# Optimization experiments

Measured on AMD Instinct MI355X. Metric: run time of the kernel, lower is better.

Reference implementation:

```python
import jax, jax.numpy as jnp
import numpy as np

B, N, D = 4, 1024, 1024      # batch, seq_len, query_dim
H, DH = 16, 64               # heads, dim_head; inner = H*DH = 1024
INNER = H * DH
SCALE = DH ** -0.5


def setup_inputs() -> dict:
    key = jax.random.key(0)
    ks = jax.random.split(key, 8)
    x = jax.random.normal(ks[0], (B, N, D), dtype=jnp.float32)
    rel_pos = jax.random.normal(ks[1], (B * H, N, N), dtype=jnp.float32)
    query_mask = jax.random.randint(ks[2], (B, N), 0, 2).astype(bool)
    context_mask = jax.random.randint(ks[3], (B, N), 0, 2).astype(bool)
    # Linear weights stored (in, out); to_q/to_kv have no bias, to_out has bias.
    Wq = jax.random.normal(ks[4], (D, INNER), dtype=jnp.float32) / np.sqrt(D)
    Wkv = jax.random.normal(ks[5], (D, 2 * INNER), dtype=jnp.float32) / np.sqrt(D)
    Wo = jax.random.normal(ks[6], (INNER, D), dtype=jnp.float32) / np.sqrt(INNER)
    bo = jax.random.normal(ks[7], (D,), dtype=jnp.float32) * 0.01
    return {"x": x, "rel_pos": rel_pos, "query_mask": query_mask,
            "context_mask": context_mask, "Wq": Wq, "Wkv": Wkv, "Wo": Wo, "bo": bo}


def reference(x, rel_pos, query_mask, context_mask, Wq, Wkv, Wo, bo):
    # Self-attention (context = x)
    q = x @ Wq                                 # [B, N, INNER]
    kv = x @ Wkv                               # [B, N, 2*INNER]
    k, v = jnp.split(kv, 2, axis=-1)
    # (b n (h d)) -> (b h n d)
    split_heads = lambda t: t.reshape(B, N, H, DH).transpose(0, 2, 1, 3)
    q, k, v = map(split_heads, (q, k, v))
    sim = jnp.einsum('bhid,bhjd->bhij', q, k) * SCALE
    sim = sim + rel_pos.reshape(B, H, N, N)
    neg = -jnp.finfo(sim.dtype).max
    # query_mask: (b i) -> mask rows; context_mask: (b j) -> mask cols
    sim = jnp.where(query_mask[:, None, :, None], sim, neg)
    sim = jnp.where(context_mask[:, None, None, :], sim, neg)
    attn = jax.nn.softmax(sim, axis=-1)
    out = jnp.einsum('bhij,bhjd->bhid', attn, v)    # [B, H, N, DH]
    out = out.transpose(0, 2, 1, 3).reshape(B, N, INNER)
    return out @ Wo + bo
```

## Files before the change

### kernel.cpp

```cpp
#include <hip/hip_runtime.h>


#define NEGMAX 3.402823466e+38f

typedef short short8 __attribute__((ext_vector_type(8)));
typedef float f32x4 __attribute__((ext_vector_type(4)));

__device__ __forceinline__ unsigned short f2bf(float f) {
  unsigned int u = __float_as_uint(f);
  u += 0x7FFFu + ((u >> 16) & 1u);
  return (unsigned short)(u >> 16);
}

__device__ __forceinline__ void stage16(const void* g, void* lds_base, int lane) {
#if __has_builtin(__builtin_amdgcn_global_load_lds)
  __builtin_amdgcn_global_load_lds(
      (const __attribute__((address_space(1))) unsigned int*)g,
      (__attribute__((address_space(3))) unsigned int*)lds_base, 16, 0, 0);
#else
  *(int4*)((char*)lds_base + lane * 16) = *(const int4*)g;
#endif
}

__global__ void cast_x_k(const float* __restrict__ x, unsigned short* __restrict__ xb) {
  int i = (blockIdx.x * 256 + threadIdx.x) * 4;
  float4 v = *(const float4*)(x + i);
  ushort4 o;
  o.x = f2bf(v.x); o.y = f2bf(v.y); o.z = f2bf(v.z); o.w = f2bf(v.w);
  *(ushort4*)(xb + i) = o;
}

__global__ __launch_bounds__(256) void tcast_k(const float* __restrict__ src, int ldsrc,
                                               unsigned short* __restrict__ dst) {
  __shared__ float T[64][65];
  const int n0 = blockIdx.x * 64, d0 = blockIdx.y * 64;
  const int tx = threadIdx.x & 63, ty = threadIdx.x >> 6;
#pragma unroll
  for (int k = 0; k < 16; ++k) {
    int dl = k * 4 + ty;
    T[dl][tx] = src[(size_t)(d0 + dl) * ldsrc + n0 + tx];
  }
  __syncthreads();
#pragma unroll
  for (int k = 0; k < 16; ++k) {
    int nl = k * 4 + ty;
    dst[(size_t)(n0 + nl) * 1024 + d0 + tx] = f2bf(T[tx][nl]);
  }
}

__global__ __launch_bounds__(256) void gemm_bt_k(
    const unsigned short* __restrict__ A, const unsigned short* __restrict__ Bt,
    unsigned short* __restrict__ qws, unsigned short* __restrict__ kws,
    unsigned short* __restrict__ vtws) {
  constexpr int K = 1024;
  constexpr int NKB = K / 32;
  __shared__ alignas(16) unsigned short As[128 * 32];
  __shared__ alignas(16) unsigned short Bs[128 * 32];
  const int tid = threadIdx.x;
  const int lane = tid & 63, w = tid >> 6;
  const int quad = lane >> 4, lanelo = lane & 15;
  const int tRow = blockIdx.y * 128, tCol = blockIdx.x * 128;
  const int wr = (w >> 1) * 64, wc = (w & 1) * 64;
  const char* AgB = (const char*)(A + (size_t)tRow * K);
  const char* BgB = (const char*)(Bt + (size_t)tCol * K);
  const int c0 = tid, c1 = tid + 256;
  const size_t a0off = (size_t)(c0 >> 2) * 2048 + (c0 & 3) * 16;
  const size_t a1off = (size_t)(c1 >> 2) * 2048 + (c1 & 3) * 16;
  char* ldsA0 = (char*)As + w * 1024;
  char* ldsA1 = (char*)As + 4096 + w * 1024;
  char* ldsB0 = (char*)Bs + w * 1024;
  char* ldsB1 = (char*)Bs + 4096 + w * 1024;

  f32x4 acc[4][4];
#pragma unroll
  for (int i = 0; i < 4; ++i)
#pragma unroll
    for (int j = 0; j < 4; ++j) acc[i][j] = (f32x4){0.f, 0.f, 0.f, 0.f};

  for (int kb = 0; kb < NKB; ++kb) {
    if (kb) __syncthreads();
    const size_t ko = (size_t)kb * 64;
    stage16(AgB + a0off + ko, ldsA0, lane);
    stage16(AgB + a1off + ko, ldsA1, lane);
    stage16(BgB + a0off + ko, ldsB0, lane);
    stage16(BgB + a1off + ko, ldsB1, lane);
    __syncthreads();

    short8 af[4], bf[4];
#pragma unroll
    for (int i = 0; i < 4; ++i)
      af[i] = *(const short8*)(As + (wr + i * 16 + lanelo) * 32 + quad * 8);
#pragma unroll
    for (int j = 0; j < 4; ++j)
      bf[j] = *(const short8*)(Bs + (wc + j * 16 + lanelo) * 32 + quad * 8);
#pragma unroll
    for (int i = 0; i < 4; ++i)
#pragma unroll
      for (int j = 0; j < 4; ++j)
        acc[i][j] = __builtin_amdgcn_mfma_f32_16x16x32_bf16(af[i], bf[j], acc[i][j], 0, 0, 0);
  }

#pragma unroll
  for (int i = 0; i < 4; ++i) {
    int row = tRow + wr + i * 16 + quad * 4;
    int b_ = row >> 10;
    int npos = row & 1023;
#pragma unroll
    for (int j = 0; j < 4; ++j) {
      int col = tCol + wc + j * 16 + lanelo;
      if (col < 2048) {
        unsigned short* dst = (col < 1024) ? qws : kws;
        int c = col & 1023;
        int hh = c >> 6, dh = c & 63;
        size_t base = ((size_t)(b_ * 16 + hh) * 1024 + npos) * 64 + dh;
#pragma unroll
        for (int r = 0; r < 4; ++r) dst[base + (size_t)r * 64] = f2bf(acc[i][j][r]);
      } else {
        int c = col - 2048;
        ushort4 pk;
        pk.x = f2bf(acc[i][j][0]);
        pk.y = f2bf(acc[i][j][1]);
        pk.z = f2bf(acc[i][j][2]);
        pk.w = f2bf(acc[i][j][3]);
        *(ushort4*)&vtws[((size_t)(b_ * 16 + (c >> 6)) * 64 + (c & 63)) * 1024 + npos] = pk;
      }
    }
  }
}

__global__ __launch_bounds__(256) void gemm64_k(
    const unsigned short* __restrict__ A, const unsigned short* __restrict__ Bt,
    const float* __restrict__ bias, float* __restrict__ Cout) {
  constexpr int K = 1024;
  constexpr int NKB = K / 32;
  __shared__ alignas(16) unsigned short As[64 * 32];
  __shared__ alignas(16) unsigned short Bs[64 * 32];
  const int tid = threadIdx.x;
  const int lane = tid & 63, w = tid >> 6;
  const int quad = lane >> 4, lanelo = lane & 15;
  const int tRow = blockIdx.y * 64, tCol = blockIdx.x * 64;
  const char* AgB = (const char*)(A + (size_t)tRow * K);
  const char* BgB = (const char*)(Bt + (size_t)tCol * K);
  const size_t aoff = (size_t)(tid >> 2) * 2048 + (tid & 3) * 16;
  char* ldsA = (char*)As + w * 1024;
  char* ldsB = (char*)Bs + w * 1024;

  f32x4 acc[4];
#pragma unroll
  for (int j = 0; j < 4; ++j) acc[j] = (f32x4){0.f, 0.f, 0.f, 0.f};

  for (int kb = 0; kb < NKB; ++kb) {
    if (kb) __syncthreads();
    const size_t ko = (size_t)kb * 64;
    stage16(AgB + aoff + ko, ldsA, lane);
    stage16(BgB + aoff + ko, ldsB, lane);
    __syncthreads();

    short8 af = *(const short8*)(As + (w * 16 + lanelo) * 32 + quad * 8);
#pragma unroll
    for (int j = 0; j < 4; ++j) {
      short8 bf = *(const short8*)(Bs + (j * 16 + lanelo) * 32 + quad * 8);
      acc[j] = __builtin_amdgcn_mfma_f32_16x16x32_bf16(af, bf, acc[j], 0, 0, 0);
    }
  }

  const int row = tRow + w * 16 + quad * 4;
#pragma unroll
  for (int j = 0; j < 4; ++j) {
    int col = tCol + j * 16 + lanelo;
    float bv = bias[col];
#pragma unroll
    for (int r = 0; r < 4; ++r)
      Cout[(size_t)(row + r) * 1024 + col] = acc[j][r] + bv;
  }
}

__global__ __launch_bounds__(256)
__attribute__((amdgpu_waves_per_eu(4, 4)))
void attn_k(
    const unsigned short* __restrict__ q_ws, const unsigned short* __restrict__ k_ws,
    const unsigned short* __restrict__ vt_ws, const float* __restrict__ rel,
    const int* __restrict__ qmask, const int* __restrict__ cmask,
    unsigned short* __restrict__ aout) {
  constexpr float SCALE = 0.125f;
  __shared__ alignas(16) unsigned short Kl[2 * 64 * 64];
  __shared__ alignas(16) unsigned short Pl[4 * 16 * 72];
  __shared__ float cml[1024];

  const int tid = threadIdx.x;
  const int w = tid >> 6, lane = tid & 63;
  const int quad = lane >> 4, lanelo = lane & 15;

  const int flat = blockIdx.y * 16 + blockIdx.x;
  const int virt = (flat & 7) * 128 + (flat >> 3);
  const int bh = virt >> 4, qblk = virt & 15;
  const int b_ = bh >> 4, h = bh & 15;
  const int qrow0 = qblk * 64 + w * 16;

  const unsigned short* kg = k_ws + (size_t)bh * 65536;
  const unsigned short* vg = vt_ws + (size_t)bh * 65536;
  const float* relg = rel + ((size_t)bh * 1024 + qrow0) * 1024;
  unsigned short* pw = Pl + w * 16 * 72;

  const int srow = lane >> 3;
  const int sp = lane & 7;
  const int spx = ((sp ^ srow) << 4);
#define STAGE_K(buf, key0n)                                                     \
  {                                                                             \
    _Pragma("unroll")                                                           \
    for (int i_ = 0; i_ < 2; ++i_) {                                            \
      int row_ = w * 16 + i_ * 8 + srow;                                        \
      stage16((const char*)kg + (size_t)((key0n) + row_) * 128 + spx,           \
              (char*)Kl + (buf) * 8192 + w * 2048 + i_ * 1024, lane);           \
    }                                                                           \
  }

  STAGE_K(0, 0);

  for (int i = tid; i < 1024; i += 256)
    cml[i] = (cmask[b_ * 1024 + i] != 0) ? 1.f : 0.f;

  const unsigned short* qg = q_ws + ((size_t)bh * 1024 + qrow0) * 64;
  short8 qf0 = *(const short8*)(qg + (size_t)lanelo * 64 + quad * 8);
  short8 qf1 = *(const short8*)(qg + (size_t)lanelo * 64 + 32 + quad * 8);

  float qmv[4];
#pragma unroll
  for (int r = 0; r < 4; ++r)
    qmv[r] = (qmask[b_ * 1024 + qrow0 + quad * 4 + r] != 0) ? 1.f : 0.f;

  f32x4 o[4];
#pragma unroll
  for (int g = 0; g < 4; ++g) o[g] = (f32x4){0.f, 0.f, 0.f, 0.f};
  float m_run[4], l_run[4];
#pragma unroll
  for (int r = 0; r < 4; ++r) { m_run[r] = -NEGMAX; l_run[r] = 0.f; }

  float rl[4][4];
#pragma unroll
  for (int r = 0; r < 4; ++r)
#pragma unroll
    for (int c = 0; c < 4; ++c)
      rl[r][c] = relg[(size_t)(quad * 4 + r) * 1024 + c * 16 + lanelo];

  const int sb = lanelo & 7;

  for (int kb = 0; kb < 16; ++kb) {
    const int key0 = kb * 64;
    const int cur = kb & 1;

    __syncthreads();

    if (kb + 1 < 16) STAGE_K(cur ^ 1, key0 + 64);

    short8 vf[8];
#pragma unroll
    for (int c2 = 0; c2 < 2; ++c2)
#pragma unroll
      for (int g = 0; g < 4; ++g)
        vf[c2 * 4 + g] = *(const short8*)(vg + (size_t)(g * 16 + lanelo) * 1024 +
                                          key0 + c2 * 32 + quad * 8);

    f32x4 s[4];
#pragma unroll
    for (int c = 0; c < 4; ++c) {
      const char* kbase = (const char*)Kl + cur * 8192 + (c * 16 + lanelo) * 128;
      short8 kfa = *(const short8*)(kbase + ((quad ^ sb) << 4));
      short8 kfb = *(const short8*)(kbase + (((4 + quad) ^ sb) << 4));
      s[c] = (f32x4){0.f, 0.f, 0.f, 0.f};
      s[c] = __builtin_amdgcn_mfma_f32_16x16x32_bf16(qf0, kfa, s[c], 0, 0, 0);
      s[c] = __builtin_amdgcn_mfma_f32_16x16x32_bf16(qf1, kfb, s[c], 0, 0, 0);
    }

    float cm[4];
#pragma unroll
    for (int c = 0; c < 4; ++c) cm[c] = cml[key0 + c * 16 + lanelo];

#pragma unroll
    for (int r = 0; r < 4; ++r) {
      const bool qok = qmv[r] != 0.f;
      float x[4], mloc = -NEGMAX;
#pragma unroll
      for (int c = 0; c < 4; ++c) {
        x[c] = (qok && cm[c] != 0.f) ? s[c][r] * SCALE + rl[r][c] : -NEGMAX;
        mloc = fmaxf(mloc, x[c]);
      }
      for (int off = 1; off < 16; off <<= 1) mloc = fmaxf(mloc, __shfl_xor(mloc, off));
      float mnew = fmaxf(m_run[r], mloc);
      float alpha = __expf(m_run[r] - mnew);
      m_run[r] = mnew;
      float ps = 0.f;
      unsigned short pb[4];
#pragma unroll
      for (int c = 0; c < 4; ++c) {
        float p = __expf(x[c] - mnew);
        ps += p;
        pb[c] = f2bf(p);
      }
      for (int off = 1; off < 16; off <<= 1) ps += __shfl_xor(ps, off);
      l_run[r] = l_run[r] * alpha + ps;
#pragma unroll
      for (int g = 0; g < 4; ++g) o[g][r] *= alpha;
#pragma unroll
      for (int c = 0; c < 4; ++c) pw[(quad * 4 + r) * 72 + c * 16 + lanelo] = pb[c];
    }

    if (kb + 1 < 16) {
#pragma unroll
      for (int r = 0; r < 4; ++r)
#pragma unroll
        for (int c = 0; c < 4; ++c)
          rl[r][c] = relg[(size_t)(quad * 4 + r) * 1024 + key0 + 64 + c * 16 + lanelo];
    }

#pragma unroll
    for (int c2 = 0; c2 < 2; ++c2) {
      short8 pa = *(const short8*)((const char*)pw + lanelo * 144 + c2 * 64 + quad * 16);
#pragma unroll
      for (int g = 0; g < 4; ++g)
        o[g] = __builtin_amdgcn_mfma_f32_16x16x32_bf16(pa, vf[c2 * 4 + g], o[g], 0, 0, 0);
    }
  }
#undef STAGE_K

#pragma unroll
  for (int r = 0; r < 4; ++r) {
    float inv = 1.f / l_run[r];
    size_t row = (size_t)(b_ * 1024 + qrow0 + quad * 4 + r) * 1024;
#pragma unroll
    for (int g = 0; g < 4; ++g)
      aout[row + h * 64 + g * 16 + lanelo] = f2bf(o[g][r] * inv);
  }
}

extern "C" void kernel_launch(void* const* d_in, const int* in_sizes, int n_in,
                              void* d_out, int out_size, void* d_ws, size_t ws_size,
                              hipStream_t stream) {
  const float* x = (const float*)d_in[0];
  const float* rel = (const float*)d_in[1];
  const int* qmask = (const int*)d_in[2];
  const int* cmask = (const int*)d_in[3];
  const float* Wq = (const float*)d_in[4];
  const float* Wkv = (const float*)d_in[5];
  const float* Wo = (const float*)d_in[6];
  const float* bo = (const float*)d_in[7];
  float* out = (float*)d_out;

  char* ws = (char*)d_ws;
  const size_t MB = 1024 * 1024;
  unsigned short* w3t = (unsigned short*)(ws);
  unsigned short* wot = (unsigned short*)(ws + 6 * MB);
  unsigned short* xb  = (unsigned short*)(ws + 8 * MB);
  unsigned short* qws = (unsigned short*)(ws + 16 * MB);
  unsigned short* kws = (unsigned short*)(ws + 24 * MB);
  unsigned short* vtws = (unsigned short*)(ws + 32 * MB);
  unsigned short* aout = xb;

  cast_x_k<<<4096, 256, 0, stream>>>(x, xb);
  tcast_k<<<dim3(16, 16), 256, 0, stream>>>(Wq, 1024, w3t);
  tcast_k<<<dim3(32, 16), 256, 0, stream>>>(Wkv, 2048, w3t + (size_t)1024 * 1024);
  tcast_k<<<dim3(16, 16), 256, 0, stream>>>(Wo, 1024, wot);
  gemm_bt_k<<<dim3(24, 32), 256, 0, stream>>>(xb, w3t, qws, kws, vtws);
  attn_k<<<dim3(16, 64), 256, 0, stream>>>(qws, kws, vtws, rel, qmask, cmask, aout);
  gemm64_k<<<dim3(16, 64), 256, 0, stream>>>(aout, wot, bo, out);
}
```

Measured before the change: 487.6 us.

## Transpose S MFMA, vectorize rel_pos loads, and add lazy softmax rescaling

```diff
diff --git a/kernel.cpp b/kernel.cpp
--- a/kernel.cpp
+++ b/kernel.cpp
@@ -185,7 +185,7 @@
   constexpr float SCALE = 0.125f;
   __shared__ alignas(16) unsigned short Kl[2 * 64 * 64];
   __shared__ alignas(16) unsigned short Pl[4 * 16 * 72];
-  __shared__ float cml[1024];
+  __shared__ float rbias[1024];
 
   const int tid = threadIdx.x;
   const int w = tid >> 6, lane = tid & 63;
@@ -203,8 +203,7 @@
   unsigned short* pw = Pl + w * 16 * 72;
 
   const int srow = lane >> 3;
-  const int sp = lane & 7;
-  const int spx = ((sp ^ srow) << 4);
+  const int spx = (((lane & 7) ^ srow) << 4);
 #define STAGE_K(buf, key0n)                                                     \
   {                                                                             \
     _Pragma("unroll")                                                           \
@@ -218,30 +217,23 @@
   STAGE_K(0, 0);
 
   for (int i = tid; i < 1024; i += 256)
-    cml[i] = (cmask[b_ * 1024 + i] != 0) ? 1.f : 0.f;
+    rbias[i] = (cmask[b_ * 1024 + i] != 0) ? 0.f : -NEGMAX;
 
   const unsigned short* qg = q_ws + ((size_t)bh * 1024 + qrow0) * 64;
   short8 qf0 = *(const short8*)(qg + (size_t)lanelo * 64 + quad * 8);
   short8 qf1 = *(const short8*)(qg + (size_t)lanelo * 64 + 32 + quad * 8);
 
-  float qmv[4];
-#pragma unroll
-  for (int r = 0; r < 4; ++r)
-    qmv[r] = (qmask[b_ * 1024 + qrow0 + quad * 4 + r] != 0) ? 1.f : 0.f;
+  const bool qok = qmask[b_ * 1024 + qrow0 + lanelo] != 0;
 
   f32x4 o[4];
 #pragma unroll
   for (int g = 0; g < 4; ++g) o[g] = (f32x4){0.f, 0.f, 0.f, 0.f};
-  float m_run[4], l_run[4];
-#pragma unroll
-  for (int r = 0; r < 4; ++r) { m_run[r] = -NEGMAX; l_run[r] = 0.f; }
-
-  float rl[4][4];
-#pragma unroll
-  for (int r = 0; r < 4; ++r)
-#pragma unroll
-    for (int c = 0; c < 4; ++c)
-      rl[r][c] = relg[(size_t)(quad * 4 + r) * 1024 + c * 16 + lanelo];
+  float m_run = -NEGMAX, l_run = 0.f;
+
+  f32x4 rl[4];
+#pragma unroll
+  for (int c = 0; c < 4; ++c)
+    rl[c] = *(const f32x4*)(relg + (size_t)lanelo * 1024 + c * 16 + quad * 4);
 
   const int sb = lanelo & 7;
 
@@ -250,7 +242,6 @@
     const int cur = kb & 1;
 
     __syncthreads();
-
     if (kb + 1 < 16) STAGE_K(cur ^ 1, key0 + 64);
 
     short8 vf[8];
@@ -268,50 +259,61 @@
       short8 kfa = *(const short8*)(kbase + ((quad ^ sb) << 4));
       short8 kfb = *(const short8*)(kbase + (((4 + quad) ^ sb) << 4));
       s[c] = (f32x4){0.f, 0.f, 0.f, 0.f};
-      s[c] = __builtin_amdgcn_mfma_f32_16x16x32_bf16(qf0, kfa, s[c], 0, 0, 0);
-      s[c] = __builtin_amdgcn_mfma_f32_16x16x32_bf16(qf1, kfb, s[c], 0, 0, 0);
-    }
-
-    float cm[4];
-#pragma unroll
-    for (int c = 0; c < 4; ++c) cm[c] = cml[key0 + c * 16 + lanelo];
-
-#pragma unroll
-    for (int r = 0; r < 4; ++r) {
-      const bool qok = qmv[r] != 0.f;
-      float x[4], mloc = -NEGMAX;
-#pragma unroll
-      for (int c = 0; c < 4; ++c) {
-        x[c] = (qok && cm[c] != 0.f) ? s[c][r] * SCALE + rl[r][c] : -NEGMAX;
-        mloc = fmaxf(mloc, x[c]);
+      s[c] = __builtin_amdgcn_mfma_f32_16x16x32_bf16(kfa, qf0, s[c], 0, 0, 0);
+      s[c] = __builtin_amdgcn_mfma_f32_16x16x32_bf16(kfb, qf1, s[c], 0, 0, 0);
+    }
+
+    f32x4 rln[4];
+    if (kb + 1 < 16) {
+#pragma unroll
+      for (int c = 0; c < 4; ++c)
+        rln[c] = *(const f32x4*)(relg + (size_t)lanelo * 1024 + key0 + 64 + c * 16 + quad * 4);
+    }
+
+    float mloc = -NEGMAX;
+#pragma unroll
+    for (int c = 0; c < 4; ++c) {
+      f32x4 rb = *(const f32x4*)(rbias + key0 + c * 16 + quad * 4);
+#pragma unroll
+      for (int r = 0; r < 4; ++r) {
+        float v = s[c][r] * SCALE + rl[c][r] + rb[r];
+        v = qok ? v : -NEGMAX;
+        s[c][r] = v;
+        mloc = fmaxf(mloc, v);
       }
-      for (int off = 1; off < 16; off <<= 1) mloc = fmaxf(mloc, __shfl_xor(mloc, off));
-      float mnew = fmaxf(m_run[r], mloc);
-      float alpha = __expf(m_run[r] - mnew);
-      m_run[r] = mnew;
-      float ps = 0.f;
-      unsigned short pb[4];
-#pragma unroll
-      for (int c = 0; c < 4; ++c) {
-        float p = __expf(x[c] - mnew);
-        ps += p;
-        pb[c] = f2bf(p);
-      }
-      for (int off = 1; off < 16; off <<= 1) ps += __shfl_xor(ps, off);
-      l_run[r] = l_run[r] * alpha + ps;
-#pragma unroll
-      for (int g = 0; g < 4; ++g) o[g][r] *= alpha;
-#pragma unroll
-      for (int c = 0; c < 4; ++c) pw[(quad * 4 + r) * 72 + c * 16 + lanelo] = pb[c];
-    }
-
-    if (kb + 1 < 16) {
-#pragma unroll
-      for (int r = 0; r < 4; ++r)
-#pragma unroll
-        for (int c = 0; c < 4; ++c)
-          rl[r][c] = relg[(size_t)(quad * 4 + r) * 1024 + key0 + 64 + c * 16 + lanelo];
-    }
+    }
+    mloc = fmaxf(mloc, __shfl_xor(mloc, 16));
+    mloc = fmaxf(mloc, __shfl_xor(mloc, 32));
+
+    if (!__all(mloc - m_run <= 8.f)) {
+      float mnew = fmaxf(m_run, mloc);
+      float alpha = __expf(m_run - mnew);
+      m_run = mnew;
+      l_run *= alpha;
+      float a4[4];
+#pragma unroll
+      for (int r = 0; r < 4; ++r) a4[r] = __shfl(alpha, quad * 4 + r, 16);
+#pragma unroll
+      for (int g = 0; g < 4; ++g)
+#pragma unroll
+        for (int r = 0; r < 4; ++r) o[g][r] *= a4[r];
+    }
+
+    float ps = 0.f;
+#pragma unroll
+    for (int c = 0; c < 4; ++c) {
+      ushort4 pk;
+      float p0 = __expf(s[c][0] - m_run);
+      float p1 = __expf(s[c][1] - m_run);
+      float p2 = __expf(s[c][2] - m_run);
+      float p3 = __expf(s[c][3] - m_run);
+      ps += (p0 + p1) + (p2 + p3);
+      pk.x = f2bf(p0); pk.y = f2bf(p1); pk.z = f2bf(p2); pk.w = f2bf(p3);
+      *(ushort4*)((char*)pw + lanelo * 144 + c * 32 + quad * 8) = pk;
+    }
+    ps += __shfl_xor(ps, 16);
+    ps += __shfl_xor(ps, 32);
+    l_run += ps;
 
 #pragma unroll
     for (int c2 = 0; c2 < 2; ++c2) {
@@ -320,16 +322,22 @@
       for (int g = 0; g < 4; ++g)
         o[g] = __builtin_amdgcn_mfma_f32_16x16x32_bf16(pa, vf[c2 * 4 + g], o[g], 0, 0, 0);
     }
+
+    if (kb + 1 < 16) {
+#pragma unroll
+      for (int c = 0; c < 4; ++c) rl[c] = rln[c];
+    }
   }
 #undef STAGE_K
 
+  float invl = 1.f / l_run;
 #pragma unroll
   for (int r = 0; r < 4; ++r) {
-    float inv = 1.f / l_run[r];
+    float iv = __shfl(invl, quad * 4 + r, 16);
     size_t row = (size_t)(b_ * 1024 + qrow0 + quad * 4 + r) * 1024;
 #pragma unroll
     for (int g = 0; g < 4; ++g)
-      aout[row + h * 64 + g * 16 + lanelo] = f2bf(o[g][r] * inv);
+      aout[row + h * 64 + g * 16 + lanelo] = f2bf(o[g][r] * iv);
   }
 }
 
```

Result: no change. 495.9 us (+1.7%).
